# Performance work log

Measured on AMD Instinct MI355X. Metric: run time of the kernel, lower is better.

## Reference

```python
import jax, jax.numpy as jnp
import numpy as np

EPS = 1e-5

def bn_relu(x, g, b):
    # BatchNorm (training-mode batch stats, biased var) + ReLU.
    # x: (..., C); per-channel stats over all leading axes.
    axes = tuple(range(x.ndim - 1))
    m = jnp.mean(x, axes, keepdims=True)
    v = jnp.var(x, axes, keepdims=True)
    return jax.nn.relu((x - m) * jax.lax.rsqrt(v + EPS) * g + b)

def knn_idx(xyz, k):
    # xyz: (B,N,3) -> (B,N,k) indices of k nearest neighbors (incl. self)
    sq = jnp.sum(xyz * xyz, -1)
    d2 = sq[:, :, None] + sq[:, None, :] - 2.0 * jnp.einsum('bnd,bmd->bnm', xyz, xyz)
    return jax.lax.top_k(-d2, k)[1]

def group(xyz, feat, k):
    # PCT sample_and_group (no FPS): gather KNN feats, concat(rel, center)
    idx = knn_idx(xyz, k)                                        # (B,N,K)
    grouped = jnp.take_along_axis(feat[:, None, :, :], idx[..., None], axis=2)  # (B,N,K,d)
    center = feat[:, :, None, :]
    return jnp.concatenate([grouped - center, jnp.broadcast_to(center, grouped.shape)], -1)

def local_op(x, W1, g1, b1, W2, g2, b2):
    # x: (B,N,K,d_i). Torch reshapes to (B*N,d_i,K): BN stats over (B,N,K).
    h = bn_relu(jnp.einsum('bnkd,od->bnko', x, W1), g1, b1)
    h = bn_relu(jnp.einsum('bnkd,od->bnko', h, W2), g2, b2)
    return jnp.max(h, axis=2)                                    # adaptive_max_pool1d(.,1)

def setup_inputs() -> dict:
    key = jax.random.key(0)
    ks = jax.random.split(key, 8)
    B, N = 8, 1024
    d_i, d_h1, d_h2, d_h3, d_o = 3, 64, 256, 512, 1024
    s = 0.02
    inp = {
        'xyz': jax.random.normal(ks[0], (B, N, d_i), jnp.float32),
        'W1': jax.random.normal(ks[1], (d_h1, d_i), jnp.float32) * s,
        'g1': jnp.ones((d_h1,), jnp.float32), 'b1': jnp.zeros((d_h1,), jnp.float32),
        'W2': jax.random.normal(ks[2], (d_h2, d_h1), jnp.float32) * s,
        'g2': jnp.ones((d_h2,), jnp.float32), 'b2': jnp.zeros((d_h2,), jnp.float32),
        'WA1': jax.random.normal(ks[3], (d_h3, d_h3), jnp.float32) * s,
        'gA1': jnp.ones((d_h3,), jnp.float32), 'bA1': jnp.zeros((d_h3,), jnp.float32),
        'WA2': jax.random.normal(ks[4], (d_h3, d_h3), jnp.float32) * s,
        'gA2': jnp.ones((d_h3,), jnp.float32), 'bA2': jnp.zeros((d_h3,), jnp.float32),
        'WB1': jax.random.normal(ks[5], (d_o, d_o), jnp.float32) * s,
        'gB1': jnp.ones((d_o,), jnp.float32), 'bB1': jnp.zeros((d_o,), jnp.float32),
        'WB2': jax.random.normal(ks[6], (d_o, d_o), jnp.float32) * s,
        'gB2': jnp.ones((d_o,), jnp.float32), 'bB2': jnp.zeros((d_o,), jnp.float32),
        'n_sample': 8,
    }
    return inp

def reference(xyz, W1, g1, b1, W2, g2, b2, WA1, gA1, bA1, WA2, gA2, bA2,
              WB1, gB1, bB1, WB2, gB2, bB2, n_sample):
    # pointwise conv-bn-relu stack on raw points (channel-last)
    h = bn_relu(jnp.einsum('bni,oi->bno', xyz, W1), g1, b1)      # (B,N,64)
    h = bn_relu(jnp.einsum('bni,oi->bno', h, W2), g2, b2)        # (B,N,256)
    g0 = group(xyz, h, n_sample)                                  # (B,N,K,512)
    l0 = local_op(g0, WA1, gA1, bA1, WA2, gA2, bA2)              # (B,N,512)
    g1_ = group(xyz, l0, n_sample)                                # (B,N,K,1024)
    l1 = local_op(g1_, WB1, gB1, bB1, WB2, gB2, bB2)             # (B,N,1024)
    return jnp.transpose(l1, (0, 2, 1))                           # (B,1024,N)
```

## Files before the change

kernel.cpp:

```cpp
#include <hip/hip_runtime.h>
#include <stdint.h>

typedef __bf16 bf8_t __attribute__((ext_vector_type(8)));
typedef float f32x4 __attribute__((ext_vector_type(4)));

#define EPSV 1e-5f

__device__ __forceinline__ float b2f(unsigned short u) {
  union { uint32_t i; float f; } v; v.i = ((uint32_t)u) << 16; return v.f;
}
__device__ __forceinline__ unsigned short f2b(float f) {
  union { float f; uint32_t i; } v; v.f = f;
  uint32_t x = v.i;
  return (unsigned short)((x + 0x7fffu + ((x >> 16) & 1u)) >> 16);
}

typedef __attribute__((address_space(1))) void gvoid;
typedef __attribute__((address_space(3))) void lvoid;
__device__ __forceinline__ void gload16(const unsigned short* g, unsigned short* l) {
  __builtin_amdgcn_global_load_lds((gvoid*)g, (lvoid*)l, 16, 0, 0);
}

__global__ __launch_bounds__(256) void cvt_f2b(const float* __restrict__ in,
                                               unsigned short* __restrict__ out, int n) {
  int gid = blockIdx.x * 256 + threadIdx.x;
  if (gid < n) out[gid] = f2b(in[gid]);
}

__global__ __launch_bounds__(256) void stage1(const float* __restrict__ xyz,
                                              const float* __restrict__ W1,
                                              float* __restrict__ y1) {
  int gid = blockIdx.x * 256 + threadIdx.x;
  int r = gid >> 6, o = gid & 63;
  float x0 = xyz[r*3+0], x1 = xyz[r*3+1], x2 = xyz[r*3+2];
  float w0 = W1[o*3+0], w1 = W1[o*3+1], w2 = W1[o*3+2];
  y1[gid] = x0*w0 + x1*w1 + x2*w2;
}

__global__ __launch_bounds__(256) void colstats(const float* __restrict__ y, int O,
                                                float* __restrict__ acc) {
  int col = blockIdx.x * 64 + (threadIdx.x & 63);
  long rbase = (long)blockIdx.y * 1024 + (threadIdx.x >> 6);
  float s = 0.f, s2 = 0.f;
  for (int i = 0; i < 256; ++i) {
    float v = y[(rbase + (long)i*4) * O + col];
    s += v; s2 += v*v;
  }
  __shared__ float red[512];
  red[threadIdx.x] = s; red[256 + threadIdx.x] = s2;
  __syncthreads();
  if (threadIdx.x < 64) {
    float S = 0.f, S2 = 0.f;
    for (int j = 0; j < 4; ++j) { S += red[threadIdx.x + 64*j]; S2 += red[256 + threadIdx.x + 64*j]; }
    atomicAdd(&acc[col], S);
    atomicAdd(&acc[O + col], S2);
  }
}

__global__ void finalize_stats(const float* __restrict__ acc, const float* __restrict__ g,
                               const float* __restrict__ b, int O, float invCount,
                               float* __restrict__ a, float* __restrict__ cc) {
  int c = blockIdx.x * 256 + threadIdx.x;
  if (c >= O) return;
  float m = acc[c] * invCount;
  float v = fmaxf(acc[O + c] * invCount - m*m, 0.f);
  float rs = rsqrtf(v + EPSV);
  float A = g[c] * rs;
  a[c] = A; cc[c] = b[c] - m * A;
}

__global__ __launch_bounds__(256) void bnrelu_cast(const float* __restrict__ y,
                                                   const float* __restrict__ a,
                                                   const float* __restrict__ cc,
                                                   int Omask,
                                                   unsigned short* __restrict__ out) {
  long base = ((long)blockIdx.x * 256 + threadIdx.x) * 8;
  int c = (int)(base & (long)Omask);
  float4 f0 = *(const float4*)(y + base);
  float4 f1 = *(const float4*)(y + base + 4);
  float4 a0 = *(const float4*)(a + c);
  float4 a1 = *(const float4*)(a + c + 4);
  float4 c0 = *(const float4*)(cc + c);
  float4 c1 = *(const float4*)(cc + c + 4);
  uint4 v;
  unsigned short* u = (unsigned short*)&v;
  u[0] = f2b(fmaxf(a0.x*f0.x + c0.x, 0.f));
  u[1] = f2b(fmaxf(a0.y*f0.y + c0.y, 0.f));
  u[2] = f2b(fmaxf(a0.z*f0.z + c0.z, 0.f));
  u[3] = f2b(fmaxf(a0.w*f0.w + c0.w, 0.f));
  u[4] = f2b(fmaxf(a1.x*f1.x + c1.x, 0.f));
  u[5] = f2b(fmaxf(a1.y*f1.y + c1.y, 0.f));
  u[6] = f2b(fmaxf(a1.z*f1.z + c1.z, 0.f));
  u[7] = f2b(fmaxf(a1.w*f1.w + c1.w, 0.f));
  *(uint4*)(out + base) = v;
}

__global__ __launch_bounds__(256) void bnrelu_inplace(unsigned short* __restrict__ y,
                                                      const float* __restrict__ a,
                                                      const float* __restrict__ cc,
                                                      int Omask) {
  long base = ((long)blockIdx.x * 256 + threadIdx.x) * 8;
  int c = (int)(base & (long)Omask);
  uint4 v = *(uint4*)(y + base);
  unsigned short* u = (unsigned short*)&v;
  float4 a0 = *(const float4*)(a + c);
  float4 a1 = *(const float4*)(a + c + 4);
  float4 c0 = *(const float4*)(cc + c);
  float4 c1 = *(const float4*)(cc + c + 4);
  float av[8] = {a0.x, a0.y, a0.z, a0.w, a1.x, a1.y, a1.z, a1.w};
  float cv[8] = {c0.x, c0.y, c0.z, c0.w, c1.x, c1.y, c1.z, c1.w};
  #pragma unroll
  for (int i = 0; i < 8; ++i) u[i] = f2b(fmaxf(av[i]*b2f(u[i]) + cv[i], 0.f));
  *(uint4*)(y + base) = v;
}

__global__ __launch_bounds__(256) void knn_kernel(const float* __restrict__ xyz,
                                                  int* __restrict__ flat_src) {
  __shared__ float px[1024], py[1024], pz[1024], sq[1024];
  int b = blockIdx.x;
  for (int i = threadIdx.x; i < 1024; i += 256) {
    float x = xyz[(b*1024 + i)*3 + 0];
    float y = xyz[(b*1024 + i)*3 + 1];
    float z = xyz[(b*1024 + i)*3 + 2];
    px[i] = x; py[i] = y; pz[i] = z; sq[i] = x*x + y*y + z*z;
  }
  __syncthreads();
  int q = blockIdx.y * 256 + threadIdx.x;
  float qx = px[q], qy = py[q], qz = pz[q], qs = sq[q];
  float bd[8]; int bi[8];
  #pragma unroll
  for (int j = 0; j < 8; ++j) { bd[j] = 3.4e38f; bi[j] = 0; }
  for (int m = 0; m < 1024; ++m) {
    float dot = qx*px[m] + qy*py[m] + qz*pz[m];
    float d2 = qs + sq[m] - 2.f*dot;
    if (d2 < bd[7]) {
      bd[7] = d2; bi[7] = m;
      #pragma unroll
      for (int j = 7; j > 0; --j) {
        if (bd[j] < bd[j-1]) {
          float td = bd[j]; bd[j] = bd[j-1]; bd[j-1] = td;
          int ti = bi[j]; bi[j] = bi[j-1]; bi[j-1] = ti;
        }
      }
    }
  }
  #pragma unroll
  for (int j = 0; j < 8; ++j) flat_src[(b*1024 + q)*8 + j] = b*1024 + bi[j];
}

__global__ __launch_bounds__(256) void wdiff(const float* __restrict__ W, int H,
                                             unsigned short* __restrict__ WD) {
  int gid = blockIdx.x * 256 + threadIdx.x;
  int o = gid / H, h = gid - o*H;
  WD[gid] = f2b(W[o*2*H + H + h] - W[o*2*H + h]);
}

union GemmSmem {
  struct { unsigned short A[128*64]; unsigned short W[128*64]; } st;
  struct { float redS[128*8]; float redS2[128*8]; } fst;
};

__global__ __launch_bounds__(256) void gemm_kernel(
    const unsigned short* __restrict__ A16,
    long strideA,
    const int* __restrict__ rowmap,
    const unsigned short* __restrict__ W, int strideW,
    int K, int O,
    const float* __restrict__ addC,
    unsigned short* __restrict__ outB,
    float* __restrict__ outF,
    float* __restrict__ statsP,
    float* __restrict__ ymax, float* __restrict__ ymin,
    float* __restrict__ statsMM)
{
  __shared__ GemmSmem sm;

  const int t = threadIdx.x;
  const int wave = t >> 6, lane = t & 63, quad = lane >> 4, lr = lane & 15;
  const int wr0 = (wave >> 1) * 64, wc0 = (wave & 1) * 64;
  const long rowBase = (long)blockIdx.x * 128;
  const int colBase = blockIdx.y * 128;

  const int lrow = lane >> 3;
  const int lchk = ((lane & 7) ^ lrow) << 3;
  const unsigned short* pa[4];
  const unsigned short* pw[4];
  #pragma unroll
  for (int j = 0; j < 4; ++j) {
    int r = wave*32 + j*8 + lrow;
    long sA = rowmap ? (long)rowmap[rowBase + r] : rowBase + r;
    pa[j] = A16 + sA * strideA + lchk;
    pw[j] = W + (long)(colBase + r) * strideW + lchk;
  }

  f32x4 acc[4][4];
  #pragma unroll
  for (int i = 0; i < 4; ++i)
    #pragma unroll
    for (int j = 0; j < 4; ++j)
      acc[i][j] = (f32x4){0.f, 0.f, 0.f, 0.f};

  for (int k0 = 0; k0 < K; k0 += 64) {
    __syncthreads();
    #pragma unroll
    for (int j = 0; j < 4; ++j) {
      gload16(pa[j] + k0, &sm.st.A[wave*2048 + j*512]);
      gload16(pw[j] + k0, &sm.st.W[wave*2048 + j*512]);
    }
    __syncthreads();

    #pragma unroll
    for (int kk = 0; kk < 2; ++kk) {
      const int coff = (((kk*4 + quad) ^ (lr & 7)) << 3);
      bf8_t af[4], bfr[4];
      #pragma unroll
      for (int s = 0; s < 4; ++s) {
        af[s]  = *(const bf8_t*)&sm.st.A[(wr0 + s*16 + lr)*64 + coff];
        bfr[s] = *(const bf8_t*)&sm.st.W[(wc0 + s*16 + lr)*64 + coff];
      }
      #pragma unroll
      for (int sr = 0; sr < 4; ++sr)
        #pragma unroll
        for (int sc = 0; sc < 4; ++sc)
          acc[sr][sc] = __builtin_amdgcn_mfma_f32_16x16x32_bf16(af[sr], bfr[sc], acc[sr][sc], 0, 0, 0);
    }
  }

  if (!ymax) {
    float s[4] = {0.f,0.f,0.f,0.f}, s2[4] = {0.f,0.f,0.f,0.f};
    #pragma unroll
    for (int sc = 0; sc < 4; ++sc) {
      int col = colBase + wc0 + sc*16 + lr;
      #pragma unroll
      for (int sr = 0; sr < 4; ++sr) {
        #pragma unroll
        for (int r = 0; r < 4; ++r) {
          long row = rowBase + wr0 + sr*16 + quad*4 + r;
          float v = acc[sr][sc][r];
          if (addC) v += addC[(row >> 3) * (long)O + col];
          if (outF) outF[row * (long)O + col] = v;
          else      outB[row * (long)O + col] = f2b(v);
          s[sc] += v; s2[sc] += v*v;
        }
      }
    }
    if (statsP) {
      __syncthreads();
      int q8 = quad + 4*(wave >> 1);
      #pragma unroll
      for (int sc = 0; sc < 4; ++sc) {
        int colL = wc0 + sc*16 + lr;
        sm.fst.redS[colL*8 + q8]  = s[sc];
        sm.fst.redS2[colL*8 + q8] = s2[sc];
      }
      __syncthreads();
      if (t < 128) {
        float S = 0.f, S2 = 0.f;
        #pragma unroll
        for (int j = 0; j < 8; ++j) { S += sm.fst.redS[t*8 + j]; S2 += sm.fst.redS2[t*8 + j]; }
        atomicAdd(&statsP[colBase + t], S);
        atomicAdd(&statsP[O + colBase + t], S2);
      }
    }
  } else {
    #pragma unroll
    for (int sc = 0; sc < 4; ++sc) {
      int col = colBase + wc0 + sc*16 + lr;
      float s = 0.f, s2v = 0.f;
      #pragma unroll
      for (int sr = 0; sr < 4; ++sr) {
        float mx = acc[sr][sc][0], mn = acc[sr][sc][0];
        s += acc[sr][sc][0]; s2v += acc[sr][sc][0]*acc[sr][sc][0];
        #pragma unroll
        for (int r = 1; r < 4; ++r) {
          float v = acc[sr][sc][r];
          mx = fmaxf(mx, v); mn = fminf(mn, v);
          s += v; s2v += v*v;
        }
        mx = fmaxf(mx, __shfl_xor(mx, 16));
        mn = fminf(mn, __shfl_xor(mn, 16));
        if ((quad & 1) == 0) {
          long orow = (long)blockIdx.x*16 + (wave >> 1)*8 + sr*2 + (quad >> 1);
          ymax[orow * O + col] = mx;
          ymin[orow * O + col] = mn;
        }
      }
      s   += __shfl_xor(s, 16);   s   += __shfl_xor(s, 32);
      s2v += __shfl_xor(s2v, 16); s2v += __shfl_xor(s2v, 32);
      if (quad == 0) {
        atomicAdd(&statsMM[col], s);
        atomicAdd(&statsMM[O + col], s2v);
      }
    }
  }
}

__global__ __launch_bounds__(256) void to_l0(const float* __restrict__ ymax,
                                             const float* __restrict__ ymin,
                                             const float* __restrict__ a, const float* __restrict__ cc,
                                             unsigned short* __restrict__ l0) {
  int gid = blockIdx.x * 256 + threadIdx.x;
  int c = gid & 511;
  float A = a[c];
  float v = (A >= 0.f) ? ymax[gid] : ymin[gid];
  l0[gid] = f2b(fmaxf(A*v + cc[c], 0.f));
}

__global__ __launch_bounds__(256) void final_out(const float* __restrict__ ymax,
                                                 const float* __restrict__ ymin,
                                                 const float* __restrict__ a, const float* __restrict__ cc,
                                                 float* __restrict__ out) {
  __shared__ float tile[32][33];
  int b = blockIdx.x, ct = blockIdx.y * 32, nt = blockIdx.z * 32;
  int tc = threadIdx.x & 31, tr = threadIdx.x >> 5;
  #pragma unroll
  for (int i = 0; i < 4; ++i) {
    int n = nt + tr + i*8;
    int c = ct + tc;
    float A = a[c];
    long idx = ((long)(b*1024 + n))*1024 + c;
    float v = (A >= 0.f) ? ymax[idx] : ymin[idx];
    tile[tr + i*8][tc] = fmaxf(A*v + cc[c], 0.f);
  }
  __syncthreads();
  #pragma unroll
  for (int i = 0; i < 4; ++i) {
    int c = ct + tr + i*8;
    int n = nt + tc;
    out[((long)(b*1024 + c))*1024 + n] = tile[tc][tr + i*8];
  }
}

extern "C" void kernel_launch(void* const* d_in, const int* in_sizes, int n_in,
                              void* d_out, int out_size, void* d_ws, size_t ws_size,
                              hipStream_t stream) {
  const float* xyz = (const float*)d_in[0];
  const float* W1  = (const float*)d_in[1];
  const float* g1  = (const float*)d_in[2];
  const float* b1  = (const float*)d_in[3];
  const float* W2  = (const float*)d_in[4];
  const float* g2  = (const float*)d_in[5];
  const float* b2  = (const float*)d_in[6];
  const float* WA1 = (const float*)d_in[7];
  const float* gA1 = (const float*)d_in[8];
  const float* bA1 = (const float*)d_in[9];
  const float* WA2 = (const float*)d_in[10];
  const float* gA2 = (const float*)d_in[11];
  const float* bA2 = (const float*)d_in[12];
  const float* WB1 = (const float*)d_in[13];
  const float* gB1 = (const float*)d_in[14];
  const float* bB1 = (const float*)d_in[15];
  const float* WB2 = (const float*)d_in[16];
  const float* gB2 = (const float*)d_in[17];
  const float* bB2 = (const float*)d_in[18];
  float* out = (float*)d_out;

  char* w = (char*)d_ws;
  const size_t MB = 1048576;

  size_t off = 0;
  auto nxt = [&](size_t bytes) { void* p = w + off; off = (off + bytes + 255) & ~(size_t)255; return p; };
  int*            flat_src = (int*)nxt(262144);
  unsigned short* W2b  = (unsigned short*)nxt(32768);
  unsigned short* WA1b = (unsigned short*)nxt(524288);
  unsigned short* WDA  = (unsigned short*)nxt(262144);
  unsigned short* WA2b = (unsigned short*)nxt(524288);
  unsigned short* WB1b = (unsigned short*)nxt(2097152);
  unsigned short* WDB  = (unsigned short*)nxt(1048576);
  unsigned short* WB2b = (unsigned short*)nxt(2097152);
  float* statsZone = (float*)nxt(27136);
  float* affZone   = (float*)nxt(27136);

  float*          yCA   = (float*)(w + 177*MB);
  float*          y1f   = (float*)(w + 193*MB);
  unsigned short* x2in  = (unsigned short*)(w + 195*MB);
  float*          y2f   = (float*)(w + 196*MB);
  unsigned short* xA1   = (unsigned short*)(w + 204*MB);
  float*          yA1f  = (float*)(w + 8*MB);
  unsigned short* xA2   = (unsigned short*)(w + 136*MB);
  float*          ymaxA = (float*)(w + 8*MB);
  float*          yminA = (float*)(w + 24*MB);
  unsigned short* l0    = (unsigned short*)(w + 40*MB);
  float*          yCB   = (float*)(w + 48*MB);
  unsigned short* yB1b  = (unsigned short*)(w + 80*MB);
  float*          ymaxB = (float*)(w + 8*MB);
  float*          yminB = (float*)(w + 40*MB);

  float* acc1  = statsZone;
  float* acc2  = statsZone + 128;
  float* accA1 = statsZone + 640;
  float* accA2 = statsZone + 1664;
  float* accB1 = statsZone + 2688;
  float* accB2 = statsZone + 4736;

  float* a1  = affZone;        float* cc1  = affZone + 64;
  float* a2  = affZone + 128;  float* cc2  = affZone + 384;
  float* aA1 = affZone + 640;  float* ccA1 = affZone + 1152;
  float* aA2 = affZone + 1664; float* ccA2 = affZone + 2176;
  float* aB1 = affZone + 2688; float* ccB1 = affZone + 3712;
  float* aB2 = affZone + 4736; float* ccB2 = affZone + 5760;

  hipMemsetAsync(statsZone, 0, 6784 * 4, stream);

  cvt_f2b<<<64, 256, 0, stream>>>(W2, W2b, 16384);
  cvt_f2b<<<1024, 256, 0, stream>>>(WA1, WA1b, 262144);
  cvt_f2b<<<1024, 256, 0, stream>>>(WA2, WA2b, 262144);
  cvt_f2b<<<4096, 256, 0, stream>>>(WB1, WB1b, 1048576);
  cvt_f2b<<<4096, 256, 0, stream>>>(WB2, WB2b, 1048576);
  wdiff<<<512, 256, 0, stream>>>(WA1, 256, WDA);
  wdiff<<<2048, 256, 0, stream>>>(WB1, 512, WDB);

  stage1<<<2048, 256, 0, stream>>>(xyz, W1, y1f);
  colstats<<<dim3(1, 8), 256, 0, stream>>>(y1f, 64, acc1);
  finalize_stats<<<1, 256, 0, stream>>>(acc1, g1, b1, 64, 1.f/8192.f, a1, cc1);
  bnrelu_cast<<<256, 256, 0, stream>>>(y1f, a1, cc1, 63, x2in);

  gemm_kernel<<<dim3(64, 2), 256, 0, stream>>>(x2in, 64, nullptr,
                                               W2b, 64, 64, 256,
                                               nullptr, nullptr, y2f, acc2, nullptr, nullptr, nullptr);
  finalize_stats<<<1, 256, 0, stream>>>(acc2, g2, b2, 256, 1.f/8192.f, a2, cc2);
  bnrelu_cast<<<1024, 256, 0, stream>>>(y2f, a2, cc2, 255, xA1);

  knn_kernel<<<dim3(8, 4), 256, 0, stream>>>(xyz, flat_src);

  gemm_kernel<<<dim3(64, 4), 256, 0, stream>>>(xA1, 256, nullptr,
                                               WDA, 256, 256, 512,
                                               nullptr, nullptr, yCA, nullptr, nullptr, nullptr, nullptr);
  gemm_kernel<<<dim3(512, 4), 256, 0, stream>>>(xA1, 256, flat_src,
                                                WA1b, 512, 256, 512,
                                                yCA, nullptr, yA1f, accA1, nullptr, nullptr, nullptr);
  finalize_stats<<<2, 256, 0, stream>>>(accA1, gA1, bA1, 512, 1.f/65536.f, aA1, ccA1);

  bnrelu_cast<<<16384, 256, 0, stream>>>(yA1f, aA1, ccA1, 511, xA2);

  gemm_kernel<<<dim3(512, 4), 256, 0, stream>>>(xA2, 512, nullptr,
                                                WA2b, 512, 512, 512,
                                                nullptr, nullptr, nullptr, nullptr, ymaxA, yminA, accA2);
  finalize_stats<<<2, 256, 0, stream>>>(accA2, gA2, bA2, 512, 1.f/65536.f, aA2, ccA2);
  to_l0<<<16384, 256, 0, stream>>>(ymaxA, yminA, aA2, ccA2, l0);

  gemm_kernel<<<dim3(64, 8), 256, 0, stream>>>(l0, 512, nullptr,
                                               WDB, 512, 512, 1024,
                                               nullptr, nullptr, yCB, nullptr, nullptr, nullptr, nullptr);
  gemm_kernel<<<dim3(512, 8), 256, 0, stream>>>(l0, 512, flat_src,
                                                WB1b, 1024, 512, 1024,
                                                yCB, yB1b, nullptr, accB1, nullptr, nullptr, nullptr);
  finalize_stats<<<4, 256, 0, stream>>>(accB1, gB1, bB1, 1024, 1.f/65536.f, aB1, ccB1);

  bnrelu_inplace<<<32768, 256, 0, stream>>>(yB1b, aB1, ccB1, 1023);

  gemm_kernel<<<dim3(512, 8), 256, 0, stream>>>(yB1b, 1024, nullptr,
                                                WB2b, 1024, 1024, 1024,
                                                nullptr, nullptr, nullptr, nullptr, ymaxB, yminB, accB2);
  finalize_stats<<<4, 256, 0, stream>>>(accB2, gB2, bB2, 1024, 1.f/65536.f, aB2, ccB2);

  final_out<<<dim3(8, 32, 32), 256, 0, stream>>>(ymaxB, yminB, aB2, ccB2, out);
}
```

Measured before the change: 1.272 ms.

## Run first local-op GEMM per point before gather, then gather in BN passes

The first conv of each local_op is linear, so it is computed once per point (N rows) instead of once per gathered neighbour row (N*K rows). The K-fold gather moves into new gstats/gbn kernels that add the centre term, accumulate BN stats and apply BN+ReLU. This removes about 8x the GEMM FLOPs in the WA1/WB1 stages, at the cost of an extra pass that reads the gathered fp32 rows to collect stats. Grid axes are also swapped so consecutive blocks walk column tiles of the same row tile, which should improve reuse of A rows in cache.

```diff
diff --git a/kernel.cpp b/kernel.cpp
--- a/kernel.cpp
+++ b/kernel.cpp
@@ -95,23 +95,61 @@
   *(uint4*)(out + base) = v;
 }
 
-__global__ __launch_bounds__(256) void bnrelu_inplace(unsigned short* __restrict__ y,
-                                                      const float* __restrict__ a,
-                                                      const float* __restrict__ cc,
-                                                      int Omask) {
-  long base = ((long)blockIdx.x * 256 + threadIdx.x) * 8;
-  int c = (int)(base & (long)Omask);
-  uint4 v = *(uint4*)(y + base);
-  unsigned short* u = (unsigned short*)&v;
-  float4 a0 = *(const float4*)(a + c);
-  float4 a1 = *(const float4*)(a + c + 4);
-  float4 c0 = *(const float4*)(cc + c);
-  float4 c1 = *(const float4*)(cc + c + 4);
-  float av[8] = {a0.x, a0.y, a0.z, a0.w, a1.x, a1.y, a1.z, a1.w};
-  float cv[8] = {c0.x, c0.y, c0.z, c0.w, c1.x, c1.y, c1.z, c1.w};
-  #pragma unroll
-  for (int i = 0; i < 8; ++i) u[i] = f2b(fmaxf(av[i]*b2f(u[i]) + cv[i], 0.f));
-  *(uint4*)(y + base) = v;
+__global__ __launch_bounds__(256) void gstats(const float* __restrict__ Z,
+                                              const float* __restrict__ C,
+                                              const int* __restrict__ fs,
+                                              int O,
+                                              float* __restrict__ acc) {
+  const int t = threadIdx.x;
+  const int cq = O >> 2;
+  const int c = (t & (cq - 1)) << 2;
+  const int rof = t / cq;
+  const int rstep = 256 / cq;
+  const long rbase = (long)blockIdx.x * 128;
+  float s0=0,s1=0,s2=0,s3=0, q0=0,q1=0,q2=0,q3=0;
+  for (int r = rof; r < 128; r += rstep) {
+    const long rr = rbase + r;
+    const long zr = (long)fs[rr] * O;
+    const long cr = (rr >> 3) * (long)O;
+    float4 z = *(const float4*)(Z + zr + c);
+    float4 y = *(const float4*)(C + cr + c);
+    float v0=z.x+y.x, v1=z.y+y.y, v2=z.z+y.z, v3=z.w+y.w;
+    s0+=v0; s1+=v1; s2+=v2; s3+=v3;
+    q0+=v0*v0; q1+=v1*v1; q2+=v2*v2; q3+=v3*v3;
+  }
+  atomicAdd(&acc[c+0], s0); atomicAdd(&acc[c+1], s1);
+  atomicAdd(&acc[c+2], s2); atomicAdd(&acc[c+3], s3);
+  atomicAdd(&acc[O+c+0], q0); atomicAdd(&acc[O+c+1], q1);
+  atomicAdd(&acc[O+c+2], q2); atomicAdd(&acc[O+c+3], q3);
+}
+
+__global__ __launch_bounds__(256) void gbn(const float* __restrict__ Z,
+                                           const float* __restrict__ C,
+                                           const int* __restrict__ fs,
+                                           const float* __restrict__ a,
+                                           const float* __restrict__ cc,
+                                           int cprShift,
+                                           unsigned short* __restrict__ out) {
+  const int O = 8 << cprShift;
+  long gid = (long)blockIdx.x * 256 + threadIdx.x;
+  long r = gid >> cprShift;
+  int c = (int)(gid & ((1 << cprShift) - 1)) << 3;
+  const long zr = (long)fs[r] * O;
+  const long cr = (r >> 3) * (long)O;
+  float4 z0 = *(const float4*)(Z + zr + c), z1 = *(const float4*)(Z + zr + c + 4);
+  float4 y0 = *(const float4*)(C + cr + c), y1 = *(const float4*)(C + cr + c + 4);
+  float4 a0 = *(const float4*)(a + c),      a1 = *(const float4*)(a + c + 4);
+  float4 b0 = *(const float4*)(cc + c),     b1 = *(const float4*)(cc + c + 4);
+  uint4 v; unsigned short* u = (unsigned short*)&v;
+  u[0] = f2b(fmaxf(a0.x*(z0.x+y0.x) + b0.x, 0.f));
+  u[1] = f2b(fmaxf(a0.y*(z0.y+y0.y) + b0.y, 0.f));
+  u[2] = f2b(fmaxf(a0.z*(z0.z+y0.z) + b0.z, 0.f));
+  u[3] = f2b(fmaxf(a0.w*(z0.w+y0.w) + b0.w, 0.f));
+  u[4] = f2b(fmaxf(a1.x*(z1.x+y1.x) + b1.x, 0.f));
+  u[5] = f2b(fmaxf(a1.y*(z1.y+y1.y) + b1.y, 0.f));
+  u[6] = f2b(fmaxf(a1.z*(z1.z+y1.z) + b1.z, 0.f));
+  u[7] = f2b(fmaxf(a1.w*(z1.w+y1.w) + b1.w, 0.f));
+  *(uint4*)(out + r*O + c) = v;
 }
 
 __global__ __launch_bounds__(256) void knn_kernel(const float* __restrict__ xyz,
@@ -178,8 +216,8 @@
   const int t = threadIdx.x;
   const int wave = t >> 6, lane = t & 63, quad = lane >> 4, lr = lane & 15;
   const int wr0 = (wave >> 1) * 64, wc0 = (wave & 1) * 64;
-  const long rowBase = (long)blockIdx.x * 128;
-  const int colBase = blockIdx.y * 128;
+  const long rowBase = (long)blockIdx.y * 128;
+  const int colBase = blockIdx.x * 128;
 
   const int lrow = lane >> 3;
   const int lchk = ((lane & 7) ^ lrow) << 3;
@@ -280,7 +318,7 @@
         mx = fmaxf(mx, __shfl_xor(mx, 16));
         mn = fminf(mn, __shfl_xor(mn, 16));
         if ((quad & 1) == 0) {
-          long orow = (long)blockIdx.x*16 + (wave >> 1)*8 + sr*2 + (quad >> 1);
+          long orow = (long)blockIdx.y*16 + (wave >> 1)*8 + sr*2 + (quad >> 1);
           ymax[orow * O + col] = mx;
           ymin[orow * O + col] = mn;
         }
@@ -376,13 +414,14 @@
   unsigned short* x2in  = (unsigned short*)(w + 195*MB);
   float*          y2f   = (float*)(w + 196*MB);
   unsigned short* xA1   = (unsigned short*)(w + 204*MB);
-  float*          yA1f  = (float*)(w + 8*MB);
-  unsigned short* xA2   = (unsigned short*)(w + 136*MB);
-  float*          ymaxA = (float*)(w + 8*MB);
-  float*          yminA = (float*)(w + 24*MB);
-  unsigned short* l0    = (unsigned short*)(w + 40*MB);
-  float*          yCB   = (float*)(w + 48*MB);
-  unsigned short* yB1b  = (unsigned short*)(w + 80*MB);
+  float*          zA    = (float*)(w + 8*MB);
+  unsigned short* xA2   = (unsigned short*)(w + 24*MB);
+  float*          ymaxA = (float*)(w + 88*MB);
+  float*          yminA = (float*)(w + 104*MB);
+  unsigned short* l0    = (unsigned short*)(w + 200*MB);
+  float*          yCB   = (float*)(w + 8*MB);
+  float*          zB    = (float*)(w + 40*MB);
+  unsigned short* yB1b  = (unsigned short*)(w + 72*MB);
   float*          ymaxB = (float*)(w + 8*MB);
   float*          yminB = (float*)(w + 40*MB);
 
@@ -415,7 +454,7 @@
   finalize_stats<<<1, 256, 0, stream>>>(acc1, g1, b1, 64, 1.f/8192.f, a1, cc1);
   bnrelu_cast<<<256, 256, 0, stream>>>(y1f, a1, cc1, 63, x2in);
 
-  gemm_kernel<<<dim3(64, 2), 256, 0, stream>>>(x2in, 64, nullptr,
+  gemm_kernel<<<dim3(2, 64), 256, 0, stream>>>(x2in, 64, nullptr,
                                                W2b, 64, 64, 256,
                                                nullptr, nullptr, y2f, acc2, nullptr, nullptr, nullptr);
   finalize_stats<<<1, 256, 0, stream>>>(acc2, g2, b2, 256, 1.f/8192.f, a2, cc2);
@@ -423,33 +462,33 @@
 
   knn_kernel<<<dim3(8, 4), 256, 0, stream>>>(xyz, flat_src);
 
-  gemm_kernel<<<dim3(64, 4), 256, 0, stream>>>(xA1, 256, nullptr,
+  gemm_kernel<<<dim3(4, 64), 256, 0, stream>>>(xA1, 256, nullptr,
                                                WDA, 256, 256, 512,
                                                nullptr, nullptr, yCA, nullptr, nullptr, nullptr, nullptr);
-  gemm_kernel<<<dim3(512, 4), 256, 0, stream>>>(xA1, 256, flat_src,
-                                                WA1b, 512, 256, 512,
-                                                yCA, nullptr, yA1f, accA1, nullptr, nullptr, nullptr);
+  gemm_kernel<<<dim3(4, 64), 256, 0, stream>>>(xA1, 256, nullptr,
+                                               WA1b, 512, 256, 512,
+                                               nullptr, nullptr, zA, nullptr, nullptr, nullptr, nullptr);
+  gstats<<<512, 256, 0, stream>>>(zA, yCA, flat_src, 512, accA1);
   finalize_stats<<<2, 256, 0, stream>>>(accA1, gA1, bA1, 512, 1.f/65536.f, aA1, ccA1);
-
-  bnrelu_cast<<<16384, 256, 0, stream>>>(yA1f, aA1, ccA1, 511, xA2);
-
-  gemm_kernel<<<dim3(512, 4), 256, 0, stream>>>(xA2, 512, nullptr,
+  gbn<<<16384, 256, 0, stream>>>(zA, yCA, flat_src, aA1, ccA1, 6, xA2);
+
+  gemm_kernel<<<dim3(4, 512), 256, 0, stream>>>(xA2, 512, nullptr,
                                                 WA2b, 512, 512, 512,
                                                 nullptr, nullptr, nullptr, nullptr, ymaxA, yminA, accA2);
   finalize_stats<<<2, 256, 0, stream>>>(accA2, gA2, bA2, 512, 1.f/65536.f, aA2, ccA2);
   to_l0<<<16384, 256, 0, stream>>>(ymaxA, yminA, aA2, ccA2, l0);
 
-  gemm_kernel<<<dim3(64, 8), 256, 0, stream>>>(l0, 512, nullptr,
+  gemm_kernel<<<dim3(8, 64), 256, 0, stream>>>(l0, 512, nullptr,
                                                WDB, 512, 512, 1024,
                                                nullptr, nullptr, yCB, nullptr, nullptr, nullptr, nullptr);
-  gemm_kernel<<<dim3(512, 8), 256, 0, stream>>>(l0, 512, flat_src,
-                                                WB1b, 1024, 512, 1024,
-                                                yCB, yB1b, nullptr, accB1, nullptr, nullptr, nullptr);
+  gemm_kernel<<<dim3(8, 64), 256, 0, stream>>>(l0, 512, nullptr,
+                                               WB1b, 1024, 512, 1024,
+                                               nullptr, nullptr, zB, nullptr, nullptr, nullptr, nullptr);
+  gstats<<<512, 256, 0, stream>>>(zB, yCB, flat_src, 1024, accB1);
   finalize_stats<<<4, 256, 0, stream>>>(accB1, gB1, bB1, 1024, 1.f/65536.f, aB1, ccB1);
-
-  bnrelu_inplace<<<32768, 256, 0, stream>>>(yB1b, aB1, ccB1, 1023);
-
-  gemm_kernel<<<dim3(512, 8), 256, 0, stream>>>(yB1b, 1024, nullptr,
+  gbn<<<32768, 256, 0, stream>>>(zB, yCB, flat_src, aB1, ccB1, 7, yB1b);
+
+  gemm_kernel<<<dim3(8, 512), 256, 0, stream>>>(yB1b, 1024, nullptr,
                                                 WB2b, 1024, 1024, 1024,
                                                 nullptr, nullptr, nullptr, nullptr, ymaxB, yminB, accB2);
   finalize_stats<<<4, 256, 0, stream>>>(accB2, gB2, bB2, 1024, 1.f/65536.f, aB2, ccB2);
```

Result: faster. 1.141 ms (-10.3%).
